# Optimization experiments

Measured on AMD Instinct MI355X. Metric: run time of the kernel, lower is better.

## Reference

```python
import jax, jax.numpy as jnp
import numpy as np

B, S, D = 1, 2048, 2048
H, KV, HD = 32, 8, 64
POWER = 100000.0


def _rotary(x):
    # x: [B, h, S, HD]; faithful to RotaryEncoder: freqs = pos / div_term
    rot_dim = HD // 2
    pos = jnp.arange(S, dtype=x.dtype)
    div = POWER ** (jnp.arange(0, HD, 2, dtype=x.dtype) / HD)  # [HD//2]
    freqs = pos[:, None] / div  # [S, HD//2]
    cos, sin = jnp.cos(freqs), jnp.sin(freqs)
    x_rot, x_pass = x[..., :rot_dim], x[..., rot_dim:]
    h = rot_dim // 2
    rot_half = jnp.concatenate([-x_rot[..., h:], x_rot[..., :h]], axis=-1)
    return jnp.concatenate([x_rot * cos + rot_half * sin, x_pass], axis=-1)


def setup_inputs() -> dict:
    key = jax.random.key(0)
    k1, k2, k3 = jax.random.split(key, 3)
    hidden_states = jax.random.normal(k1, (B, S, D), dtype=jnp.float32)
    op_size = H * HD + 2 * KV * HD
    Wqkv = jax.random.normal(k2, (D, op_size), dtype=jnp.float32) * 0.02
    Wo = jax.random.normal(k3, (H * HD, D), dtype=jnp.float32) * 0.02
    causal = jnp.tril(jnp.ones((S, S), dtype=bool))
    attention_mask = jnp.where(causal, 0.0, -1e9).astype(jnp.float32)[None, None]
    return {"hidden_states": hidden_states, "attention_mask": attention_mask,
            "Wqkv": Wqkv, "Wo": Wo}


def reference(hidden_states, attention_mask, Wqkv, Wo):
    groups = H // KV
    qkv = hidden_states @ Wqkv  # [B, S, op_size]
    qpos = H * HD
    q = qkv[..., :qpos].reshape(B, S, H, HD).transpose(0, 2, 1, 3)
    k = qkv[..., qpos:qpos + KV * HD].reshape(B, S, KV, HD).transpose(0, 2, 1, 3)
    v = qkv[..., qpos + KV * HD:].reshape(B, S, KV, HD).transpose(0, 2, 1, 3)
    q = _rotary(q)
    k = _rotary(k)
    k = jnp.repeat(k, groups, axis=1)  # GQA repeat_interleave -> [B, H, S, HD]
    v = jnp.repeat(v, groups, axis=1)
    scores = jnp.einsum('bhqd,bhkd->bhqk', q, k) / jnp.sqrt(jnp.float32(HD))
    scores = scores + attention_mask[..., :S]
    attn = jax.nn.softmax(scores.astype(jnp.float32), axis=-1).astype(v.dtype)
    out = jnp.einsum('bhqk,bhkd->bhqd', attn, v)
    out = out.transpose(0, 2, 1, 3).reshape(B, S, H * HD)
    return out @ Wo
```

## Files before the change

kernel.cpp:

```cpp
#include <hip/hip_runtime.h>
#include <hip/hip_bf16.h>
#include <cstdint>
#include <cstddef>

#define S_LEN 2048
#define D_MODEL 2048
#define NH 32
#define NKV 8
#define HDIM 64
#define OPSZ 3072
#define KOFF 2048
#define VOFF 2560

typedef float    floatx4 __attribute__((ext_vector_type(4)));
typedef __bf16   bf16x8  __attribute__((ext_vector_type(8)));
typedef __bf16   bf16x4  __attribute__((ext_vector_type(4)));
typedef __bf16   bf16_t;
typedef _Float16 f16_t;
typedef _Float16 f16x4   __attribute__((ext_vector_type(4)));

__device__ __forceinline__ void gld16(const void* g, void* l) {
  __builtin_amdgcn_global_load_lds((__attribute__((address_space(1))) void*)(void*)g,
                                   (__attribute__((address_space(3))) void*)l,
                                   16, 0, 0);
}

__global__ __launch_bounds__(256) void convert_x(const float* __restrict__ X,
                                                 bf16_t* __restrict__ Xb) {
  const int i = (blockIdx.x * 256 + threadIdx.x) * 4;
  const float4 v = *(const float4*)(X + i);
  bf16x4 t;
  t[0] = (bf16_t)v.x; t[1] = (bf16_t)v.y; t[2] = (bf16_t)v.z; t[3] = (bf16_t)v.w;
  *(bf16x4*)(Xb + i) = t;
}

__global__ __launch_bounds__(256) void transpose_w(const float* __restrict__ W,
                                                   bf16_t* __restrict__ Wt,
                                                   int K, int N) {
  __shared__ float tile[32][33];
  const int n0 = blockIdx.x * 32, k0 = blockIdx.y * 32;
  const int tx = threadIdx.x & 31, ty = threadIdx.x >> 5;
#pragma unroll
  for (int i = 0; i < 32; i += 8)
    tile[ty + i][tx] = W[(size_t)(k0 + ty + i) * N + n0 + tx];
  __syncthreads();
#pragma unroll
  for (int i = 0; i < 32; i += 8)
    Wt[(size_t)(n0 + ty + i) * K + k0 + tx] = (bf16_t)tile[tx][ty + i];
}

#define GEMM64_CORE(A_, Bt_, K_, m0_, n0_)                                        \
  const int tid = threadIdx.x;                                                    \
  const int wave = tid >> 6;                                                      \
  const int lane = tid & 63;                                                      \
  const int lane15 = lane & 15;                                                   \
  const int quad = lane >> 4;                                                     \
  const int wm = (wave & 1) * 32;                                                 \
  const int wn = (wave >> 1) * 64;                                                \
  floatx4 acc[2][4];                                                              \
  _Pragma("unroll") for (int i = 0; i < 2; i++)                                   \
    _Pragma("unroll") for (int j = 0; j < 4; j++)                                 \
      acc[i][j] = floatx4{0.f, 0.f, 0.f, 0.f};                                    \
  {                                                                               \
    const int ca = tid;                                                           \
    const int ara = ca >> 2, aca = (ca & 3) * 8;                                  \
    const int cb0 = tid, cb1 = tid + 256;                                         \
    const int br0 = cb0 >> 2, bc0 = (cb0 & 3) * 8;                                \
    const int br1 = cb1 >> 2, bc1 = (cb1 & 3) * 8;                                \
    bf16_t* lA  = &As[(wave * 64) * 8];                                           \
    bf16_t* lB0 = &Bs[(wave * 64) * 8];                                           \
    bf16_t* lB1 = &Bs[(256 + wave * 64) * 8];                                     \
    for (int k0 = 0; k0 < (K_); k0 += 32) {                                       \
      __syncthreads();                                                            \
      gld16((A_)  + (size_t)((m0_) + ara) * (K_) + k0 + aca, lA);                 \
      gld16((Bt_) + (size_t)((n0_) + br0) * (K_) + k0 + bc0, lB0);                \
      gld16((Bt_) + (size_t)((n0_) + br1) * (K_) + k0 + bc1, lB1);                \
      __syncthreads();                                                            \
      bf16x8 af[2], bfr[4];                                                       \
      _Pragma("unroll") for (int mi = 0; mi < 2; mi++)                            \
        af[mi] = *(const bf16x8*)&As[(wm + mi * 16 + lane15) * 32 + quad * 8];    \
      _Pragma("unroll") for (int ni = 0; ni < 4; ni++)                            \
        bfr[ni] = *(const bf16x8*)&Bs[(wn + ni * 16 + lane15) * 32 + quad * 8];   \
      _Pragma("unroll") for (int mi = 0; mi < 2; mi++)                            \
        _Pragma("unroll") for (int ni = 0; ni < 4; ni++)                          \
          acc[mi][ni] = __builtin_amdgcn_mfma_f32_16x16x32_bf16(af[mi], bfr[ni],  \
                                                                acc[mi][ni], 0, 0, 0); \
    }                                                                             \
  }

#define QSCALE 0.18033688011112042f
__global__ __launch_bounds__(256, 2)
void gemm_qkv_rope(const bf16_t* __restrict__ A, const bf16_t* __restrict__ Bt,
                   bf16_t* __restrict__ Qr, bf16_t* __restrict__ Kr,
                   f16_t* __restrict__ VtG) {
  __shared__ bf16_t As[64 * 32];
  __shared__ bf16_t Bs[128 * 32];
  const int m0 = blockIdx.y * 64;
  const int n0 = blockIdx.x * 128;
  GEMM64_CORE(A, Bt, D_MODEL, m0, n0)

  const int colbase = n0 + wn;
  const int s0 = m0 + wm;

  if (colbase < VOFF) {
    const bool isQ = (colbase < KOFF);
    const float k2 = 0.51905126483f;
    const float pj0 = exp2f(-(float)lane15 * k2);
    const float pj1 = pj0 * 0.0031622776601684f;
    bf16_t* dst = isQ ? (Qr + ((size_t)(colbase >> 6) * S_LEN) * HDIM)
                      : (Kr + ((size_t)((colbase - KOFF) >> 6) * S_LEN) * HDIM);
    const float qs = isQ ? QSCALE : 1.0f;
#pragma unroll
    for (int mi = 0; mi < 2; mi++) {
#pragma unroll
      for (int r = 0; r < 4; r++) {
        const int s = s0 + mi * 16 + quad * 4 + r;
        const float sf = (float)s;
        float s0s, s0c, s1s, s1c;
        __sincosf(sf * pj0, &s0s, &s0c);
        __sincosf(sf * pj1, &s1s, &s1c);
        const float x0 = acc[mi][0][r], x1 = acc[mi][1][r];
        bf16_t* row = dst + (size_t)s * HDIM + lane15;
        row[0]  = (bf16_t)((x0 * s0c - x1 * s0s) * qs);
        row[16] = (bf16_t)((x1 * s1c + x0 * s1s) * qs);
        row[32] = (bf16_t)(acc[mi][2][r] * qs);
        row[48] = (bf16_t)(acc[mi][3][r] * qs);
      }
    }
  } else {
    const int kvv = (colbase - VOFF) >> 6;
    f16_t* dst = VtG + (size_t)kvv * HDIM * S_LEN;
#pragma unroll
    for (int mi = 0; mi < 2; mi++) {
      const int s = s0 + mi * 16 + quad * 4;
#pragma unroll
      for (int ni = 0; ni < 4; ni++) {
        const int d = ni * 16 + lane15;
        f16x4 tv;
#pragma unroll
        for (int r = 0; r < 4; r++) tv[r] = (f16_t)acc[mi][ni][r];
        *(f16x4*)&dst[(size_t)d * S_LEN + s] = tv;
      }
    }
  }
}

__global__ __launch_bounds__(256, 2)
void gemm_bt_f32out(const bf16_t* __restrict__ A, const bf16_t* __restrict__ Bt,
                    float* __restrict__ C, int M, int N, int K) {
  __shared__ bf16_t As[64 * 32];
  __shared__ bf16_t Bs[128 * 32];
  const int m0 = blockIdx.y * 64;
  const int n0 = blockIdx.x * 128;
  GEMM64_CORE(A, Bt, K, m0, n0)

#pragma unroll
  for (int mi = 0; mi < 2; mi++)
#pragma unroll
    for (int r = 0; r < 4; r++) {
      const int row = m0 + wm + mi * 16 + quad * 4 + r;
#pragma unroll
      for (int ni = 0; ni < 4; ni++) {
        const int col = n0 + wn + ni * 16 + lane15;
        C[(size_t)row * N + col] = acc[mi][ni][r];
      }
    }
}

#define KST 72
#define VST 68
__global__ __launch_bounds__(256, 4)
void flash_kernel(const bf16_t* __restrict__ Qr, const bf16_t* __restrict__ Kr,
                  const f16_t* __restrict__ VtG, bf16_t* __restrict__ attn) {
  __shared__ bf16_t Ks[64 * KST];
  __shared__ f16_t  Vt[64 * VST];

  const int tid = threadIdx.x;
  const int wave = tid >> 6;
  const int lane = tid & 63;
  const int lane15 = lane & 15;
  const int quad = lane >> 4;
  const int bx = blockIdx.x;
  const int h = bx & 31;
  const int qblk = 31 - (bx >> 5);
  const int q0 = qblk * 64;
  const int rq = q0 + wave * 16;
  const int kv = h >> 2;
  const size_t kbase = (size_t)kv * S_LEN * HDIM;
  const size_t vbase = (size_t)kv * HDIM * S_LEN;

  bf16x8 aq[2];
#pragma unroll
  for (int kt = 0; kt < 2; kt++)
    aq[kt] = *(const bf16x8*)&Qr[((size_t)h * S_LEN + rq + lane15) * HDIM + kt * 32 + quad * 8];

  float m_run = -1e30f, l_run = 0.f;
  floatx4 o[4];
#pragma unroll
  for (int dt = 0; dt < 4; dt++) o[dt] = floatx4{0.f, 0.f, 0.f, 0.f};

  const int nk = qblk + 1;
  for (int t = 0; t < nk; ++t) {
    const int p0 = t * 64;
    __syncthreads();
#pragma unroll
    for (int i = 0; i < 2; i++) {
      const int c = tid + i * 256;
      const int r = c >> 3, col = (c & 7) * 8;
      *(bf16x8*)&Ks[r * KST + col] = *(const bf16x8*)&Kr[kbase + (size_t)(p0 + r) * HDIM + col];
    }
#pragma unroll
    for (int i = 0; i < 4; i++) {
      const int c = tid + i * 256;
      const int d = c >> 4, col = (c & 15) * 4;
      *(f16x4*)&Vt[d * VST + col] = *(const f16x4*)&VtG[vbase + (size_t)d * S_LEN + p0 + col];
    }
    __syncthreads();

    floatx4 sc[4];
#pragma unroll
    for (int nt = 0; nt < 4; nt++) sc[nt] = floatx4{0.f, 0.f, 0.f, 0.f};
#pragma unroll
    for (int kt = 0; kt < 2; kt++) {
      bf16x8 ak[4];
#pragma unroll
      for (int nt = 0; nt < 4; nt++)
        ak[nt] = *(const bf16x8*)&Ks[(nt * 16 + lane15) * KST + kt * 32 + quad * 8];
#pragma unroll
      for (int nt = 0; nt < 4; nt++)
        sc[nt] = __builtin_amdgcn_mfma_f32_16x16x32_bf16(ak[nt], aq[kt], sc[nt], 0, 0, 0);
    }

    if (p0 + 63 > rq) {
#pragma unroll
      for (int nt = 0; nt < 4; nt++)
#pragma unroll
        for (int r = 0; r < 4; r++) {
          const int kpos = p0 + nt * 16 + quad * 4 + r;
          const int qrow = rq + lane15;
          if (kpos > qrow) sc[nt][r] = -1e30f;
        }
    }

    float mt = fmaxf(fmaxf(sc[0][0], sc[0][1]), fmaxf(sc[0][2], sc[0][3]));
#pragma unroll
    for (int nt = 1; nt < 4; nt++)
#pragma unroll
      for (int r = 0; r < 4; r++) mt = fmaxf(mt, sc[nt][r]);
    mt = fmaxf(mt, __shfl_xor(mt, 16));
    mt = fmaxf(mt, __shfl_xor(mt, 32));
    const float mnew = fmaxf(m_run, mt);
    const float alpha = exp2f(m_run - mnew);
    m_run = mnew;
    float rs = 0.f;
    f16x4 ph[4];
#pragma unroll
    for (int nt = 0; nt < 4; nt++) {
      f16x4 pv;
#pragma unroll
      for (int r = 0; r < 4; r++) {
        const float p = exp2f(sc[nt][r] - mnew);
        rs += p;
        pv[r] = (f16_t)p;
      }
      ph[nt] = pv;
    }
    rs += __shfl_xor(rs, 16);
    rs += __shfl_xor(rs, 32);
    l_run = l_run * alpha + rs;
#pragma unroll
    for (int dt = 0; dt < 4; dt++)
#pragma unroll
      for (int r = 0; r < 4; r++) o[dt][r] *= alpha;

#pragma unroll
    for (int kt4 = 0; kt4 < 4; kt4++) {
      f16x4 av[4];
#pragma unroll
      for (int dt = 0; dt < 4; dt++)
        av[dt] = *(const f16x4*)&Vt[(dt * 16 + lane15) * VST + kt4 * 16 + quad * 4];
#pragma unroll
      for (int dt = 0; dt < 4; dt++)
        o[dt] = __builtin_amdgcn_mfma_f32_16x16x16f16(av[dt], ph[kt4], o[dt], 0, 0, 0);
    }
  }

  const float inv = 1.0f / l_run;
  const int s = rq + lane15;
#pragma unroll
  for (int dt = 0; dt < 4; dt++) {
    bf16x4 tv;
#pragma unroll
    for (int r = 0; r < 4; r++) tv[r] = (bf16_t)(o[dt][r] * inv);
    *(bf16x4*)&attn[(size_t)s * D_MODEL + h * HDIM + dt * 16 + quad * 4] = tv;
  }
}

extern "C" void kernel_launch(void* const* d_in, const int* in_sizes, int n_in,
                              void* d_out, int out_size, void* d_ws, size_t ws_size,
                              hipStream_t stream) {
  (void)in_sizes; (void)n_in; (void)out_size; (void)ws_size;
  const float* hidden = (const float*)d_in[0];
  const float* Wqkv = (const float*)d_in[2];
  const float* Wo   = (const float*)d_in[3];
  float* out = (float*)d_out;

  char* ws = (char*)d_ws;
  size_t off = 0;
  auto alloc = [&](size_t bytes) -> void* {
    void* p = ws + off;
    off += (bytes + 255) & ~(size_t)255;
    return p;
  };
  bf16_t* Xb    = (bf16_t*)alloc((size_t)S_LEN * D_MODEL * 2);
  bf16_t* WqkvT = (bf16_t*)alloc((size_t)OPSZ * D_MODEL * 2);
  bf16_t* WoT   = (bf16_t*)alloc((size_t)D_MODEL * D_MODEL * 2);
  bf16_t* Qr    = (bf16_t*)alloc((size_t)NH * S_LEN * HDIM * 2);
  bf16_t* Kr    = (bf16_t*)alloc((size_t)NKV * S_LEN * HDIM * 2);
  f16_t*  VtG   = (f16_t*) alloc((size_t)NKV * HDIM * S_LEN * 2);
  bf16_t* attn  = (bf16_t*)alloc((size_t)S_LEN * D_MODEL * 2);

  convert_x<<<(S_LEN * D_MODEL) / 1024, 256, 0, stream>>>(hidden, Xb);
  transpose_w<<<dim3(OPSZ / 32, D_MODEL / 32), 256, 0, stream>>>(Wqkv, WqkvT, D_MODEL, OPSZ);
  transpose_w<<<dim3(D_MODEL / 32, D_MODEL / 32), 256, 0, stream>>>(Wo, WoT, D_MODEL, D_MODEL);
  gemm_qkv_rope<<<dim3(OPSZ / 128, S_LEN / 64), 256, 0, stream>>>(Xb, WqkvT, Qr, Kr, VtG);
  flash_kernel<<<dim3(32 * NH), 256, 0, stream>>>(Qr, Kr, VtG, attn);
  gemm_bt_f32out<<<dim3(D_MODEL / 128, S_LEN / 64), 256, 0, stream>>>(attn, WoT, out, S_LEN, D_MODEL, D_MODEL);
}
```

Baseline: 236.7 us.

## Double-buffer K/V tiles in flash attention and widen GEMM K-step to 64

The flash kernel now keeps two LDS buffers for the K and V tiles. It prefetches the next tile while computing on the current one, which drops one barrier per iteration and lets global loads overlap the MFMA and softmax work. The shared GEMM core now loads two 32-wide K panels per barrier pair, halving the synchronisation count per K. The cost is doubled LDS per block in all kernels, which may limit occupancy, plus more registers held for in-flight loads.

Result: faster. 223.9 us (-5.4%).

```diff
diff --git a/kernel.cpp b/kernel.cpp
--- a/kernel.cpp
+++ b/kernel.cpp
@@ -62,29 +62,37 @@
     _Pragma("unroll") for (int j = 0; j < 4; j++)                                 \
       acc[i][j] = floatx4{0.f, 0.f, 0.f, 0.f};                                    \
   {                                                                               \
-    const int ca = tid;                                                           \
-    const int ara = ca >> 2, aca = (ca & 3) * 8;                                  \
-    const int cb0 = tid, cb1 = tid + 256;                                         \
-    const int br0 = cb0 >> 2, bc0 = (cb0 & 3) * 8;                                \
-    const int br1 = cb1 >> 2, bc1 = (cb1 & 3) * 8;                                \
-    bf16_t* lA  = &As[(wave * 64) * 8];                                           \
-    bf16_t* lB0 = &Bs[(wave * 64) * 8];                                           \
-    bf16_t* lB1 = &Bs[(256 + wave * 64) * 8];                                     \
-    for (int k0 = 0; k0 < (K_); k0 += 32) {                                       \
+                                                  \
+    const int ca0 = tid, ca1 = tid + 256;                                         \
+    const int apan0 = ca0 >> 8, ar0 = (ca0 & 255) >> 2, ac0 = (ca0 & 3) * 8;      \
+    const int apan1 = ca1 >> 8, ar1 = (ca1 & 255) >> 2, ac1 = (ca1 & 3) * 8;      \
+                  \
+    int bpan[4], br[4], bc[4];                                                    \
+    _Pragma("unroll") for (int i = 0; i < 4; i++) {                               \
+      const int c = tid + i * 256;                                                \
+      bpan[i] = c >> 9; br[i] = (c & 511) >> 2; bc[i] = (c & 3) * 8;              \
+    }                                                                             \
+    bf16_t* lA0 = &As[(wave * 64) * 8];                                           \
+    bf16_t* lA1 = &As[(256 + wave * 64) * 8];                                     \
+    for (int k0 = 0; k0 < (K_); k0 += 64) {                                       \
       __syncthreads();                                                            \
-      gld16((A_)  + (size_t)((m0_) + ara) * (K_) + k0 + aca, lA);                 \
-      gld16((Bt_) + (size_t)((n0_) + br0) * (K_) + k0 + bc0, lB0);                \
-      gld16((Bt_) + (size_t)((n0_) + br1) * (K_) + k0 + bc1, lB1);                \
+      gld16((A_) + (size_t)((m0_) + ar0) * (K_) + k0 + apan0 * 32 + ac0, lA0);    \
+      gld16((A_) + (size_t)((m0_) + ar1) * (K_) + k0 + apan1 * 32 + ac1, lA1);    \
+      _Pragma("unroll") for (int i = 0; i < 4; i++)                               \
+        gld16((Bt_) + (size_t)((n0_) + br[i]) * (K_) + k0 + bpan[i] * 32 + bc[i], \
+              &Bs[(i * 256 + wave * 64) * 8]);                                    \
       __syncthreads();                                                            \
-      bf16x8 af[2], bfr[4];                                                       \
-      _Pragma("unroll") for (int mi = 0; mi < 2; mi++)                            \
-        af[mi] = *(const bf16x8*)&As[(wm + mi * 16 + lane15) * 32 + quad * 8];    \
-      _Pragma("unroll") for (int ni = 0; ni < 4; ni++)                            \
-        bfr[ni] = *(const bf16x8*)&Bs[(wn + ni * 16 + lane15) * 32 + quad * 8];   \
-      _Pragma("unroll") for (int mi = 0; mi < 2; mi++)                            \
+      _Pragma("unroll") for (int kt = 0; kt < 2; kt++) {                          \
+        bf16x8 af[2], bfr[4];                                                     \
+        _Pragma("unroll") for (int mi = 0; mi < 2; mi++)                          \
+          af[mi] = *(const bf16x8*)&As[kt * 2048 + (wm + mi * 16 + lane15) * 32 + quad * 8]; \
         _Pragma("unroll") for (int ni = 0; ni < 4; ni++)                          \
-          acc[mi][ni] = __builtin_amdgcn_mfma_f32_16x16x32_bf16(af[mi], bfr[ni],  \
-                                                                acc[mi][ni], 0, 0, 0); \
+          bfr[ni] = *(const bf16x8*)&Bs[kt * 4096 + (wn + ni * 16 + lane15) * 32 + quad * 8]; \
+        _Pragma("unroll") for (int mi = 0; mi < 2; mi++)                          \
+          _Pragma("unroll") for (int ni = 0; ni < 4; ni++)                        \
+            acc[mi][ni] = __builtin_amdgcn_mfma_f32_16x16x32_bf16(af[mi], bfr[ni],\
+                                                                  acc[mi][ni], 0, 0, 0); \
+      }                                                                           \
     }                                                                             \
   }
 
@@ -93,8 +101,8 @@
 void gemm_qkv_rope(const bf16_t* __restrict__ A, const bf16_t* __restrict__ Bt,
                    bf16_t* __restrict__ Qr, bf16_t* __restrict__ Kr,
                    f16_t* __restrict__ VtG) {
-  __shared__ bf16_t As[64 * 32];
-  __shared__ bf16_t Bs[128 * 32];
+  __shared__ bf16_t As[2 * 64 * 32];
+  __shared__ bf16_t Bs[2 * 128 * 32];
   const int m0 = blockIdx.y * 64;
   const int n0 = blockIdx.x * 128;
   GEMM64_CORE(A, Bt, D_MODEL, m0, n0)
@@ -148,8 +156,8 @@
 __global__ __launch_bounds__(256, 2)
 void gemm_bt_f32out(const bf16_t* __restrict__ A, const bf16_t* __restrict__ Bt,
                     float* __restrict__ C, int M, int N, int K) {
-  __shared__ bf16_t As[64 * 32];
-  __shared__ bf16_t Bs[128 * 32];
+  __shared__ bf16_t As[2 * 64 * 32];
+  __shared__ bf16_t Bs[2 * 128 * 32];
   const int m0 = blockIdx.y * 64;
   const int n0 = blockIdx.x * 128;
   GEMM64_CORE(A, Bt, K, m0, n0)
@@ -172,8 +180,8 @@
 __global__ __launch_bounds__(256, 4)
 void flash_kernel(const bf16_t* __restrict__ Qr, const bf16_t* __restrict__ Kr,
                   const f16_t* __restrict__ VtG, bf16_t* __restrict__ attn) {
-  __shared__ bf16_t Ks[64 * KST];
-  __shared__ f16_t  Vt[64 * VST];
+  __shared__ bf16_t Ks[2][64 * KST];
+  __shared__ f16_t  Vt[2][64 * VST];
 
   const int tid = threadIdx.x;
   const int wave = tid >> 6;
@@ -189,6 +197,9 @@
   const size_t kbase = (size_t)kv * S_LEN * HDIM;
   const size_t vbase = (size_t)kv * HDIM * S_LEN;
 
+  const int kr_ = tid >> 3, kc_ = (tid & 7) * 8;
+  const int vd_ = tid >> 4, vc_ = (tid & 15) * 4;
+
   bf16x8 aq[2];
 #pragma unroll
   for (int kt = 0; kt < 2; kt++)
@@ -200,22 +211,37 @@
   for (int dt = 0; dt < 4; dt++) o[dt] = floatx4{0.f, 0.f, 0.f, 0.f};
 
   const int nk = qblk + 1;
+
+#pragma unroll
+  for (int i = 0; i < 2; i++) {
+    const int r = kr_ + i * 32;
+    *(bf16x8*)&Ks[0][r * KST + kc_] = *(const bf16x8*)&Kr[kbase + (size_t)r * HDIM + kc_];
+  }
+#pragma unroll
+  for (int i = 0; i < 4; i++) {
+    const int d = vd_ + i * 16;
+    *(f16x4*)&Vt[0][d * VST + vc_] = *(const f16x4*)&VtG[vbase + (size_t)d * S_LEN + vc_];
+  }
+
   for (int t = 0; t < nk; ++t) {
     const int p0 = t * 64;
+    const int cur = t & 1;
     __syncthreads();
-#pragma unroll
-    for (int i = 0; i < 2; i++) {
-      const int c = tid + i * 256;
-      const int r = c >> 3, col = (c & 7) * 8;
-      *(bf16x8*)&Ks[r * KST + col] = *(const bf16x8*)&Kr[kbase + (size_t)(p0 + r) * HDIM + col];
-    }
-#pragma unroll
-    for (int i = 0; i < 4; i++) {
-      const int c = tid + i * 256;
-      const int d = c >> 4, col = (c & 15) * 4;
-      *(f16x4*)&Vt[d * VST + col] = *(const f16x4*)&VtG[vbase + (size_t)d * S_LEN + p0 + col];
-    }
-    __syncthreads();
+
+    if (t + 1 < nk) {
+      const int nxt = cur ^ 1;
+      const int pn = p0 + 64;
+#pragma unroll
+      for (int i = 0; i < 2; i++) {
+        const int r = kr_ + i * 32;
+        *(bf16x8*)&Ks[nxt][r * KST + kc_] = *(const bf16x8*)&Kr[kbase + (size_t)(pn + r) * HDIM + kc_];
+      }
+#pragma unroll
+      for (int i = 0; i < 4; i++) {
+        const int d = vd_ + i * 16;
+        *(f16x4*)&Vt[nxt][d * VST + vc_] = *(const f16x4*)&VtG[vbase + (size_t)d * S_LEN + pn + vc_];
+      }
+    }
 
     floatx4 sc[4];
 #pragma unroll
@@ -225,7 +251,7 @@
       bf16x8 ak[4];
 #pragma unroll
       for (int nt = 0; nt < 4; nt++)
-        ak[nt] = *(const bf16x8*)&Ks[(nt * 16 + lane15) * KST + kt * 32 + quad * 8];
+        ak[nt] = *(const bf16x8*)&Ks[cur][(nt * 16 + lane15) * KST + kt * 32 + quad * 8];
 #pragma unroll
       for (int nt = 0; nt < 4; nt++)
         sc[nt] = __builtin_amdgcn_mfma_f32_16x16x32_bf16(ak[nt], aq[kt], sc[nt], 0, 0, 0);
@@ -278,7 +304,7 @@
       f16x4 av[4];
 #pragma unroll
       for (int dt = 0; dt < 4; dt++)
-        av[dt] = *(const f16x4*)&Vt[(dt * 16 + lane15) * VST + kt4 * 16 + quad * 4];
+        av[dt] = *(const f16x4*)&Vt[cur][(dt * 16 + lane15) * VST + kt4 * 16 + quad * 4];
 #pragma unroll
       for (int dt = 0; dt < 4; dt++)
         o[dt] = __builtin_amdgcn_mfma_f32_16x16x16f16(av[dt], ph[kt4], o[dt], 0, 0, 0);
```
